# Performance work log

Hardware: AMD Instinct MI355X
Metric: run time of the kernel (lower is better)

The kernel has to match this reference:

```python
import jax, jax.numpy as jnp
import numpy as np

D = 4096


def ste_sign(v):
    # forward: sign(v); backward: identity (straight-through)
    return v + jax.lax.stop_gradient(jnp.sign(v) - v)


def setup_inputs() -> dict:
    key = jax.random.key(0)
    ks = jax.random.split(key, 7)
    B, T = 2, 4096
    x = jax.random.normal(ks[0], (B, T, D), dtype=jnp.float32)
    role_write = jax.random.normal(ks[1], (D,), dtype=jnp.float32) * 0.02
    role_read = jax.random.normal(ks[2], (D,), dtype=jnp.float32) * 0.02
    # nn.Linear(D, 1): weight (1, D) stored here as (D,), bias scalar (1,)
    lim = 1.0 / np.sqrt(D)
    wg_w = jax.random.uniform(ks[3], (D,), dtype=jnp.float32, minval=-lim, maxval=lim)
    wg_b = jax.random.uniform(ks[4], (1,), dtype=jnp.float32, minval=-lim, maxval=lim)
    rg_w = jax.random.uniform(ks[5], (D,), dtype=jnp.float32, minval=-lim, maxval=lim)
    rg_b = jax.random.uniform(ks[6], (1,), dtype=jnp.float32, minval=-lim, maxval=lim)
    return {"x": x, "role_write": role_write, "role_read": role_read,
            "wg_w": wg_w, "wg_b": wg_b, "rg_w": rg_w, "rg_b": rg_b}


def reference(x, role_write, role_read, wg_w, wg_b, rg_w, rg_b):
    # ---- write: gated sign-bind facts, causal bundle via cumsum over T ----
    signs = ste_sign(x)                                  # (B,T,D)
    facts = signs * ste_sign(role_write)                 # bind with write role
    w_gate = jax.nn.sigmoid(jnp.einsum('btd,d->bt', x, wg_w) + wg_b[0])
    gated_facts = facts * w_gate[..., None]
    memory = jnp.cumsum(gated_facts, axis=1)             # (B,T,D) causal bundle
    # ---- read: unbind memory with query, gated residual add ----
    query = signs * ste_sign(role_read)
    retrieved = ste_sign(memory) * query
    r_gate = jax.nn.sigmoid(jnp.einsum('btd,d->bt', x, rg_w) + rg_b[0])
    return x + r_gate[..., None] * retrieved
```

## Files before the change

kernel.cpp:

```cpp
#include <hip/hip_runtime.h>
#include <math.h>


#define T_LEN 4096
#define D_LEN 4096
#define NC 64
#define TC (T_LEN / NC)
#define D4 (D_LEN / 4)

__device__ __forceinline__ float fsgn(float v) {
    return (v > 0.f) ? 1.f : ((v < 0.f) ? -1.f : 0.f);
}
__device__ __forceinline__ double dsgn(double v) {
    return (v > 0.) ? 1. : ((v < 0.) ? -1. : 0.);
}

__global__ __launch_bounds__(256) void gates_kernel(
    const float* __restrict__ x,
    const float* __restrict__ wg_w, const float* __restrict__ wg_b,
    const float* __restrict__ rg_w, const float* __restrict__ rg_b,
    double* __restrict__ wgate, double* __restrict__ rgate)
{
    const int row = blockIdx.x;
    const float4* xr = (const float4*)(x + (size_t)row * D_LEN);
    const float4* w4 = (const float4*)wg_w;
    const float4* r4 = (const float4*)rg_w;

    double dw = 0., dr = 0.;
    for (int i = threadIdx.x; i < D4; i += 256) {
        float4 v = xr[i];
        float4 a = w4[i];
        float4 b = r4[i];
        dw += (double)v.x * a.x + (double)v.y * a.y
            + (double)v.z * a.z + (double)v.w * a.w;
        dr += (double)v.x * b.x + (double)v.y * b.y
            + (double)v.z * b.z + (double)v.w * b.w;
    }
    for (int off = 32; off > 0; off >>= 1) {
        dw += __shfl_down(dw, off);
        dr += __shfl_down(dr, off);
    }
    __shared__ double sdw[4], sdr[4];
    const int wid = threadIdx.x >> 6;
    if ((threadIdx.x & 63) == 0) { sdw[wid] = dw; sdr[wid] = dr; }
    __syncthreads();
    if (threadIdx.x == 0) {
        double zw = sdw[0] + sdw[1] + sdw[2] + sdw[3] + (double)wg_b[0];
        double zr = sdr[0] + sdr[1] + sdr[2] + sdr[3] + (double)rg_b[0];
        wgate[row] = 1. / (1. + exp(-zw));
        rgate[row] = 1. / (1. + exp(-zr));
    }
}

__global__ __launch_bounds__(256) void partial_kernel(
    const float* __restrict__ x,
    const double* __restrict__ wgate,
    double* __restrict__ partial)
{
    const int b = blockIdx.z;
    const int c = blockIdx.y;
    const int d4 = blockIdx.x * 256 + threadIdx.x;

    __shared__ double wsm[TC];
    if (threadIdx.x < TC)
        wsm[threadIdx.x] = wgate[b * T_LEN + c * TC + threadIdx.x];
    __syncthreads();

    const float4* x4 = (const float4*)x;
    size_t base = ((size_t)b * T_LEN + (size_t)c * TC) * D4 + d4;

    double ax = 0., ay = 0., az = 0., aw = 0.;
    #pragma unroll 4
    for (int i = 0; i < TC; ++i) {
        float4 v = x4[base + (size_t)i * D4];
        double w = wsm[i];
        ax += (double)fsgn(v.x) * w;
        ay += (double)fsgn(v.y) * w;
        az += (double)fsgn(v.z) * w;
        aw += (double)fsgn(v.w) * w;
    }
    double* p = partial + (((size_t)(b * NC + c)) * D4 + d4) * 4;
    p[0] = ax; p[1] = ay; p[2] = az; p[3] = aw;
}

__global__ __launch_bounds__(256) void final_kernel(
    const float* __restrict__ x,
    const double* __restrict__ wgate, const double* __restrict__ rgate,
    const float* __restrict__ role_w, const float* __restrict__ role_r,
    const double* __restrict__ partial,
    float* __restrict__ out)
{
    const int b = blockIdx.z;
    const int c = blockIdx.y;
    const int d4 = blockIdx.x * 256 + threadIdx.x;

    __shared__ double wsm[TC], rsm[TC];
    if (threadIdx.x < TC) {
        wsm[threadIdx.x] = wgate[b * T_LEN + c * TC + threadIdx.x];
        rsm[threadIdx.x] = rgate[b * T_LEN + c * TC + threadIdx.x];
    }
    __syncthreads();

    float4 rw = ((const float4*)role_w)[d4];
    float4 rr = ((const float4*)role_r)[d4];
    const double kx = (double)(fsgn(rw.x) * fsgn(rr.x));
    const double ky = (double)(fsgn(rw.y) * fsgn(rr.y));
    const double kz = (double)(fsgn(rw.z) * fsgn(rr.z));
    const double kw = (double)(fsgn(rw.w) * fsgn(rr.w));

    double ax = 0., ay = 0., az = 0., aw = 0.;
    for (int c2 = 0; c2 < c; ++c2) {
        const double* p = partial + (((size_t)(b * NC + c2)) * D4 + d4) * 4;
        ax += p[0]; ay += p[1]; az += p[2]; aw += p[3];
    }

    const float4* x4 = (const float4*)x;
    float4* o4 = (float4*)out;
    size_t base = ((size_t)b * T_LEN + (size_t)c * TC) * D4 + d4;

    #pragma unroll 4
    for (int i = 0; i < TC; ++i) {
        float4 v = x4[base + (size_t)i * D4];
        double w = wsm[i];
        double r = rsm[i];
        double sx = (double)fsgn(v.x), sy = (double)fsgn(v.y);
        double sz = (double)fsgn(v.z), sw2 = (double)fsgn(v.w);
        ax += sx * w; ay += sy * w; az += sz * w; aw += sw2 * w;
        float4 o;
        o.x = (float)((double)v.x + r * kx * dsgn(ax) * sx);
        o.y = (float)((double)v.y + r * ky * dsgn(ay) * sy);
        o.z = (float)((double)v.z + r * kz * dsgn(az) * sz);
        o.w = (float)((double)v.w + r * kw * dsgn(aw) * sw2);
        o4[base + (size_t)i * D4] = o;
    }
}

extern "C" void kernel_launch(void* const* d_in, const int* in_sizes, int n_in,
                              void* d_out, int out_size, void* d_ws, size_t ws_size,
                              hipStream_t stream) {
    const float* x      = (const float*)d_in[0];
    const float* role_w = (const float*)d_in[1];
    const float* role_r = (const float*)d_in[2];
    const float* wg_w   = (const float*)d_in[3];
    const float* wg_b   = (const float*)d_in[4];
    const float* rg_w   = (const float*)d_in[5];
    const float* rg_b   = (const float*)d_in[6];
    float* out = (float*)d_out;

    const int B = in_sizes[0] / (T_LEN * D_LEN);
    const int BT = B * T_LEN;

    double* wgate   = (double*)d_ws;
    double* rgate   = wgate + BT;
    double* partial = rgate + BT;

    gates_kernel<<<BT, 256, 0, stream>>>(x, wg_w, wg_b, rg_w, rg_b, wgate, rgate);

    dim3 grid(D4 / 256, NC, B);
    partial_kernel<<<grid, 256, 0, stream>>>(x, wgate, partial);
    final_kernel<<<grid, 256, 0, stream>>>(x, wgate, rgate, role_w, role_r,
                                           partial, out);
}
```

Measured before the change: 105.2 us.

## Fuse gate computation with chunk partials and add a separate prefix-scan kernel

Merges the gate dot-product and per-chunk partial sums into one kernel so each 32-row slab of x is read while it is likely still in cache. A dedicated prefix kernel replaces the quadratic per-block loop over earlier chunk partials in the final kernel. The chunk size is halved. Part of the final arithmetic is moved from double to float. Risks include fewer blocks in the fused kernel (NC*B = 256 blocks of 512 threads), a larger partial/prefix workspace, and slight precision changes in the output.

```diff
diff --git a/kernel.cpp b/kernel.cpp
--- a/kernel.cpp
+++ b/kernel.cpp
@@ -4,8 +4,8 @@
 
 #define T_LEN 4096
 #define D_LEN 4096
-#define NC 64
-#define TC (T_LEN / NC)
+#define TC 32
+#define NC (T_LEN / TC)
 #define D4 (D_LEN / 4)
 
 __device__ __forceinline__ float fsgn(float v) {
@@ -15,123 +15,131 @@
     return (v > 0.) ? 1. : ((v < 0.) ? -1. : 0.);
 }
 
-__global__ __launch_bounds__(256) void gates_kernel(
+__global__ __launch_bounds__(512) void gates_partial_kernel(
     const float* __restrict__ x,
     const float* __restrict__ wg_w, const float* __restrict__ wg_b,
     const float* __restrict__ rg_w, const float* __restrict__ rg_b,
-    double* __restrict__ wgate, double* __restrict__ rgate)
+    double* __restrict__ wgate, double* __restrict__ rgate,
+    double* __restrict__ partial)
 {
-    const int row = blockIdx.x;
-    const float4* xr = (const float4*)(x + (size_t)row * D_LEN);
+    const int c = blockIdx.x;
+    const int b = blockIdx.y;
+    const int tid = threadIdx.x;
+
+    __shared__ double wsm[TC];
+
+    const int r   = tid >> 4;
+    const int sub = tid & 15;
+    const float4* x4 = (const float4*)x;
     const float4* w4 = (const float4*)wg_w;
-    const float4* r4 = (const float4*)rg_w;
+    const float4* g4 = (const float4*)rg_w;
+    const size_t rowbase = ((size_t)b * T_LEN + (size_t)c * TC + r) * D4;
 
     double dw = 0., dr = 0.;
-    for (int i = threadIdx.x; i < D4; i += 256) {
-        float4 v = xr[i];
-        float4 a = w4[i];
-        float4 b = r4[i];
+    #pragma unroll 4
+    for (int k = sub; k < D4; k += 16) {
+        float4 v = x4[rowbase + k];
+        float4 a = w4[k];
+        float4 g = g4[k];
         dw += (double)v.x * a.x + (double)v.y * a.y
             + (double)v.z * a.z + (double)v.w * a.w;
-        dr += (double)v.x * b.x + (double)v.y * b.y
-            + (double)v.z * b.z + (double)v.w * b.w;
+        dr += (double)v.x * g.x + (double)v.y * g.y
+            + (double)v.z * g.z + (double)v.w * g.w;
     }
-    for (int off = 32; off > 0; off >>= 1) {
-        dw += __shfl_down(dw, off);
-        dr += __shfl_down(dr, off);
+    #pragma unroll
+    for (int off = 8; off >= 1; off >>= 1) {
+        dw += __shfl_down(dw, off, 16);
+        dr += __shfl_down(dr, off, 16);
     }
-    __shared__ double sdw[4], sdr[4];
-    const int wid = threadIdx.x >> 6;
-    if ((threadIdx.x & 63) == 0) { sdw[wid] = dw; sdr[wid] = dr; }
+    if (sub == 0) {
+        double wg = 1. / (1. + exp(-(dw + (double)wg_b[0])));
+        double rg = 1. / (1. + exp(-(dr + (double)rg_b[0])));
+        wsm[r] = wg;
+        const int row = b * T_LEN + c * TC + r;
+        wgate[row] = wg;
+        rgate[row] = rg;
+    }
     __syncthreads();
-    if (threadIdx.x == 0) {
-        double zw = sdw[0] + sdw[1] + sdw[2] + sdw[3] + (double)wg_b[0];
-        double zr = sdr[0] + sdr[1] + sdr[2] + sdr[3] + (double)rg_b[0];
-        wgate[row] = 1. / (1. + exp(-zw));
-        rgate[row] = 1. / (1. + exp(-zr));
+
+    const size_t slab = ((size_t)b * T_LEN + (size_t)c * TC) * D4;
+    for (int dd = tid; dd < D4; dd += 512) {
+        double ax = 0., ay = 0., az = 0., aw = 0.;
+        #pragma unroll 8
+        for (int i = 0; i < TC; ++i) {
+            float4 v = x4[slab + (size_t)i * D4 + dd];
+            double w = wsm[i];
+            ax += (double)fsgn(v.x) * w;
+            ay += (double)fsgn(v.y) * w;
+            az += (double)fsgn(v.z) * w;
+            aw += (double)fsgn(v.w) * w;
+        }
+        double* p = partial + (((size_t)(b * NC + c)) * D4 + dd) * 4;
+        p[0] = ax; p[1] = ay; p[2] = az; p[3] = aw;
     }
 }
 
-__global__ __launch_bounds__(256) void partial_kernel(
+__global__ __launch_bounds__(256) void prefix_kernel(
+    const double* __restrict__ partial, double* __restrict__ prefix)
+{
+    const int m = blockIdx.x * 256 + threadIdx.x;
+    const int b = blockIdx.y;
+    double s = 0.;
+    #pragma unroll 4
+    for (int c = 0; c < NC; ++c) {
+        size_t idx = ((size_t)(b * NC + c)) * (D4 * 4) + m;
+        double v = partial[idx];
+        prefix[idx] = s;
+        s += v;
+    }
+}
+
+__global__ __launch_bounds__(256) void final_kernel(
     const float* __restrict__ x,
-    const double* __restrict__ wgate,
-    double* __restrict__ partial)
+    const double* __restrict__ wgate, const double* __restrict__ rgate,
+    const float* __restrict__ role_w, const float* __restrict__ role_r,
+    const double* __restrict__ prefix,
+    float* __restrict__ out)
 {
     const int b = blockIdx.z;
     const int c = blockIdx.y;
     const int d4 = blockIdx.x * 256 + threadIdx.x;
 
     __shared__ double wsm[TC];
-    if (threadIdx.x < TC)
-        wsm[threadIdx.x] = wgate[b * T_LEN + c * TC + threadIdx.x];
-    __syncthreads();
-
-    const float4* x4 = (const float4*)x;
-    size_t base = ((size_t)b * T_LEN + (size_t)c * TC) * D4 + d4;
-
-    double ax = 0., ay = 0., az = 0., aw = 0.;
-    #pragma unroll 4
-    for (int i = 0; i < TC; ++i) {
-        float4 v = x4[base + (size_t)i * D4];
-        double w = wsm[i];
-        ax += (double)fsgn(v.x) * w;
-        ay += (double)fsgn(v.y) * w;
-        az += (double)fsgn(v.z) * w;
-        aw += (double)fsgn(v.w) * w;
-    }
-    double* p = partial + (((size_t)(b * NC + c)) * D4 + d4) * 4;
-    p[0] = ax; p[1] = ay; p[2] = az; p[3] = aw;
-}
-
-__global__ __launch_bounds__(256) void final_kernel(
-    const float* __restrict__ x,
-    const double* __restrict__ wgate, const double* __restrict__ rgate,
-    const float* __restrict__ role_w, const float* __restrict__ role_r,
-    const double* __restrict__ partial,
-    float* __restrict__ out)
-{
-    const int b = blockIdx.z;
-    const int c = blockIdx.y;
-    const int d4 = blockIdx.x * 256 + threadIdx.x;
-
-    __shared__ double wsm[TC], rsm[TC];
+    __shared__ float rsm[TC];
     if (threadIdx.x < TC) {
         wsm[threadIdx.x] = wgate[b * T_LEN + c * TC + threadIdx.x];
-        rsm[threadIdx.x] = rgate[b * T_LEN + c * TC + threadIdx.x];
+        rsm[threadIdx.x] = (float)rgate[b * T_LEN + c * TC + threadIdx.x];
     }
     __syncthreads();
 
     float4 rw = ((const float4*)role_w)[d4];
     float4 rr = ((const float4*)role_r)[d4];
-    const double kx = (double)(fsgn(rw.x) * fsgn(rr.x));
-    const double ky = (double)(fsgn(rw.y) * fsgn(rr.y));
-    const double kz = (double)(fsgn(rw.z) * fsgn(rr.z));
-    const double kw = (double)(fsgn(rw.w) * fsgn(rr.w));
+    const float kx = fsgn(rw.x) * fsgn(rr.x);
+    const float ky = fsgn(rw.y) * fsgn(rr.y);
+    const float kz = fsgn(rw.z) * fsgn(rr.z);
+    const float kw = fsgn(rw.w) * fsgn(rr.w);
 
-    double ax = 0., ay = 0., az = 0., aw = 0.;
-    for (int c2 = 0; c2 < c; ++c2) {
-        const double* p = partial + (((size_t)(b * NC + c2)) * D4 + d4) * 4;
-        ax += p[0]; ay += p[1]; az += p[2]; aw += p[3];
-    }
+    const double* p = prefix + (((size_t)(b * NC + c)) * D4 + d4) * 4;
+    double ax = p[0], ay = p[1], az = p[2], aw = p[3];
 
     const float4* x4 = (const float4*)x;
     float4* o4 = (float4*)out;
-    size_t base = ((size_t)b * T_LEN + (size_t)c * TC) * D4 + d4;
+    const size_t slab = ((size_t)b * T_LEN + (size_t)c * TC) * D4 + d4;
 
     #pragma unroll 4
     for (int i = 0; i < TC; ++i) {
-        float4 v = x4[base + (size_t)i * D4];
+        float4 v = x4[slab + (size_t)i * D4];
         double w = wsm[i];
-        double r = rsm[i];
-        double sx = (double)fsgn(v.x), sy = (double)fsgn(v.y);
-        double sz = (double)fsgn(v.z), sw2 = (double)fsgn(v.w);
-        ax += sx * w; ay += sy * w; az += sz * w; aw += sw2 * w;
+        float rf = rsm[i];
+        float sx = fsgn(v.x), sy = fsgn(v.y), sz = fsgn(v.z), sw2 = fsgn(v.w);
+        ax += (double)sx * w; ay += (double)sy * w;
+        az += (double)sz * w; aw += (double)sw2 * w;
         float4 o;
-        o.x = (float)((double)v.x + r * kx * dsgn(ax) * sx);
-        o.y = (float)((double)v.y + r * ky * dsgn(ay) * sy);
-        o.z = (float)((double)v.z + r * kz * dsgn(az) * sz);
-        o.w = (float)((double)v.w + r * kw * dsgn(aw) * sw2);
-        o4[base + (size_t)i * D4] = o;
+        o.x = v.x + rf * kx * (float)dsgn(ax) * sx;
+        o.y = v.y + rf * ky * (float)dsgn(ay) * sy;
+        o.z = v.z + rf * kz * (float)dsgn(az) * sz;
+        o.w = v.w + rf * kw * (float)dsgn(aw) * sw2;
+        o4[slab + (size_t)i * D4] = o;
     }
 }
 
@@ -153,11 +161,16 @@
     double* wgate   = (double*)d_ws;
     double* rgate   = wgate + BT;
     double* partial = rgate + BT;
+    double* prefix  = partial + (size_t)B * NC * (D4 * 4);
 
-    gates_kernel<<<BT, 256, 0, stream>>>(x, wg_w, wg_b, rg_w, rg_b, wgate, rgate);
+    dim3 g12(NC, B);
+    gates_partial_kernel<<<g12, 512, 0, stream>>>(
+        x, wg_w, wg_b, rg_w, rg_b, wgate, rgate, partial);
 
-    dim3 grid(D4 / 256, NC, B);
-    partial_kernel<<<grid, 256, 0, stream>>>(x, wgate, partial);
-    final_kernel<<<grid, 256, 0, stream>>>(x, wgate, rgate, role_w, role_r,
-                                           partial, out);
+    dim3 g25((D4 * 4) / 256, B);
+    prefix_kernel<<<g25, 256, 0, stream>>>(partial, prefix);
+
+    dim3 g3(D4 / 256, NC, B);
+    final_kernel<<<g3, 256, 0, stream>>>(
+        x, wgate, rgate, role_w, role_r, prefix, out);
 }
```

After: 112.9 us. 7.3% more time.
